# Kernel tuning notes

Hardware: AMD Instinct MI355X
Metric: run time of the kernel (lower is better)

Reference implementation:

```python
import jax, jax.numpy as jnp
import numpy as np

N = 65536        # lattice nodes (256x256 grid)
E_RAND = 1_000_000  # non-self-loop causal edges (~16 per node)
T = 65           # max edge type after add_self_loops (type 1 = self loop)
FIN = 8
FOUT = 8
B = 16           # batch of spin configurations


def setup_inputs() -> dict:
    key = jax.random.key(0)
    k1, k2, k3, k4, k5, k6 = jax.random.split(key, 6)
    x = jax.random.normal(k1, (N, FIN, B), dtype=jnp.float32)
    bound = 1.0 / np.sqrt(FIN)  # matches reset_parameters uniform init
    W = jax.random.uniform(k2, (T, FOUT, FIN), jnp.float32, -bound, bound)
    b = jax.random.uniform(k3, (T, FOUT), jnp.float32, -bound, bound)
    # add_self_loops: identity edges with type 1, other types shifted to 2..T
    loops = jnp.arange(N, dtype=jnp.int32)
    src = jnp.concatenate([loops, jax.random.randint(k4, (E_RAND,), 0, N, dtype=jnp.int32)])
    tgt = jnp.concatenate([loops, jax.random.randint(k5, (E_RAND,), 0, N, dtype=jnp.int32)])
    etype = jnp.concatenate([
        jnp.ones((N,), dtype=jnp.int32),
        jax.random.randint(k6, (E_RAND,), 2, T + 1, dtype=jnp.int32),
    ])
    return {"x": x, "W": W, "b": b, "src": src, "tgt": tgt, "etype": etype}


def reference(x, W, b, src, tgt, etype):
    # Faithful to GraphConvLayer.forward (depth=None): the expanded sparse
    # weight matrix assigns a unique [FOUT,FIN] block W[t-1] to every base
    # edge (tgt,src) of type t, and torch.sparse.mm sums duplicate entries.
    Wg = W[etype - 1]                              # [E, FOUT, FIN] gather by edge type
    msg = jnp.einsum('eoi,eib->eob', Wg, x[src])   # per-edge messages [E, FOUT, B]
    y = jax.ops.segment_sum(msg, tgt, num_segments=N)       # [N, FOUT, B]
    # bias graph expanded with source_dim=1, multiplied by ones -> per-edge bias
    yb = jax.ops.segment_sum(b[etype - 1], tgt, num_segments=N)  # [N, FOUT]
    return y + yb[:, :, None]
```

## Files before the change

### kernel.cpp

```cpp
#include <hip/hip_runtime.h>


#define CAP 48
#define ROWSTRIDE 52
#define DUMMY_T 65
#define NT 66
#define BUCKETS 512
#define BNODES 128
#define WCAP 32
#define CHUNK 4096

typedef short bf16x8 __attribute__((ext_vector_type(8)));
typedef float f32x4 __attribute__((ext_vector_type(4)));

__device__ __forceinline__ unsigned f2bf(float f) {
    unsigned u = __float_as_uint(f);
    return (u + 0x7FFFu + ((u >> 16) & 1u)) >> 16;
}

__device__ __forceinline__ int qperm(int r) { return (r == 1) ? 2 : (r == 2) ? 1 : r; }

__global__ __launch_bounds__(256)
void bin_a(const float* __restrict__ x, const float* __restrict__ W,
           const int* __restrict__ rsrc, const int* __restrict__ rtgt,
           const int* __restrict__ rety,
           int* __restrict__ cnts, unsigned* __restrict__ bdata,
           uint4* __restrict__ xt, uint4* __restrict__ Wbf, int N, int ER, int nchunk) {
    __shared__ int hist[BUCKETS];
    __shared__ int curs[BUCKETS];
    int bid = blockIdx.x, tid = threadIdx.x;

    if (bid < nchunk) {
        hist[tid] = 0; hist[tid + 256] = 0;
        curs[tid] = 0; curs[tid + 256] = 0;
        __syncthreads();
        int e0 = bid * CHUNK;
        int lim = ER - e0; if (lim > CHUNK) lim = CHUNK;

        unsigned pay[4][4];
        int bb[4][4];
        int nv[4];
#pragma unroll
        for (int g = 0; g < 4; ++g) {
            int r = tid * 4 + g * 1024;
            int n = lim - r; n = n < 0 ? 0 : (n > 4 ? 4 : n);
            nv[g] = n;
            if (n == 4) {
                int4 tv = *reinterpret_cast<const int4*>(rtgt + e0 + r);
                int4 sv = *reinterpret_cast<const int4*>(rsrc + e0 + r);
                int4 qv = *reinterpret_cast<const int4*>(rety + e0 + r);
                bb[g][0] = tv.x >> 7; pay[g][0] = (unsigned)(tv.x & 127) | ((unsigned)sv.x << 7) | ((unsigned)(qv.x - 1) << 23);
                bb[g][1] = tv.y >> 7; pay[g][1] = (unsigned)(tv.y & 127) | ((unsigned)sv.y << 7) | ((unsigned)(qv.y - 1) << 23);
                bb[g][2] = tv.z >> 7; pay[g][2] = (unsigned)(tv.z & 127) | ((unsigned)sv.z << 7) | ((unsigned)(qv.z - 1) << 23);
                bb[g][3] = tv.w >> 7; pay[g][3] = (unsigned)(tv.w & 127) | ((unsigned)sv.w << 7) | ((unsigned)(qv.w - 1) << 23);
            } else {
#pragma unroll
                for (int u = 0; u < 4; ++u) {
                    if (u < n) {
                        int e = e0 + r + u;
                        int t = rtgt[e];
                        bb[g][u] = t >> 7;
                        pay[g][u] = (unsigned)(t & 127) | ((unsigned)rsrc[e] << 7)
                                  | ((unsigned)(rety[e] - 1) << 23);
                    } else { bb[g][u] = 0; pay[g][u] = 0; }
                }
            }
#pragma unroll
            for (int u = 0; u < 4; ++u)
                if (u < nv[g]) atomicAdd(&hist[bb[g][u]], 1);
        }
        __syncthreads();
        cnts[bid * BUCKETS + tid]       = min(hist[tid], WCAP);
        cnts[bid * BUCKETS + tid + 256] = min(hist[tid + 256], WCAP);
#pragma unroll
        for (int g = 0; g < 4; ++g) {
#pragma unroll
            for (int u = 0; u < 4; ++u) {
                if (u < nv[g]) {
                    int bkt = bb[g][u];
                    int pos = atomicAdd(&curs[bkt], 1);
                    if (pos < WCAP)
                        bdata[((size_t)bkt * nchunk + bid) * WCAP + pos] = pay[g][u];
                }
            }
        }
    } else if (bid < nchunk + (N * 16) / 256) {
        int p = (bid - nchunk) * 256 + tid;
        int n = p >> 4, j = p & 15;
        const float* xp = x + (size_t)n * 128 + j;
        unsigned w[4];
#pragma unroll
        for (int i = 0; i < 4; ++i)
            w[i] = f2bf(xp[(2 * i) * 16]) | (f2bf(xp[(2 * i + 1) * 16]) << 16);
        xt[p] = make_uint4(w[0], w[1], w[2], w[3]);
    } else {
        for (int i = tid; i < NT * 8; i += 256) {
            uint4 wv = make_uint4(0, 0, 0, 0);
            if (i < 65 * 8) {
                const float* wr = W + (size_t)i * 8;
                wv = make_uint4(f2bf(wr[0]) | (f2bf(wr[1]) << 16),
                                f2bf(wr[2]) | (f2bf(wr[3]) << 16),
                                f2bf(wr[4]) | (f2bf(wr[5]) << 16),
                                f2bf(wr[6]) | (f2bf(wr[7]) << 16));
            }
            Wbf[i] = wv;
        }
    }
}

__global__ __launch_bounds__(512, 8)
void build_gather(const int* __restrict__ cnts, const unsigned* __restrict__ bdata,
                  const float* __restrict__ bias, const uint4* __restrict__ xt,
                  const uint4* __restrict__ Wbf, float* __restrict__ out, int nchunk) {
    __shared__ unsigned ladj[BNODES * ROWSTRIDE];
    __shared__ int ldeg[BNODES];
    __shared__ int lnit[BNODES];
    __shared__ float blds[NT * 8];
    __shared__ float lyb[BNODES * 8];
    __shared__ int lcnt[512];
    int b = blockIdx.x, tid = threadIdx.x;

    if (tid < BNODES) ldeg[tid] = 0;
    const unsigned DUM = (unsigned)DUMMY_T << 16;
    uint4* l4 = reinterpret_cast<uint4*>(ladj);
#pragma unroll 4
    for (int i = tid; i < BNODES * ROWSTRIDE / 4; i += 512)
        l4[i] = make_uint4(DUM, DUM, DUM, DUM);
    for (int i = tid; i < NT * 8; i += 512)
        blds[i] = (i < 65 * 8) ? bias[i] : 0.f;
    for (int i = tid; i < nchunk; i += 512)
        lcnt[i] = cnts[i * BUCKETS + b];
    __syncthreads();

    const unsigned* bp = bdata + (size_t)b * nchunk * WCAP;
    int totslots = nchunk * WCAP;
    for (int s = tid; s < totslots; s += 512) {
        int c = s >> 5, k = s & 31;
        if (k < lcnt[c]) {
            unsigned p = bp[s];
            int tl = (int)(p & 127u);
            int pos = atomicAdd(&ldeg[tl], 1);
            if (pos < CAP)
                ladj[tl * ROWSTRIDE + (pos & ~3) + qperm(pos & 3)] =
                    ((p >> 7) & 0xFFFFu) | ((p >> 23) << 16);
        }
    }
    __syncthreads();

    if (tid < BNODES) {
        int node = b * BNODES + tid;
        int d = ldeg[tid]; if (d > CAP) d = CAP;
        ladj[tid * ROWSTRIDE + (d & ~3) + qperm(d & 3)] = (unsigned)node;
        lnit[tid] = (d + 4) >> 2;
    }
    __syncthreads();

#pragma unroll
    for (int base = 0; base < BNODES * 8; base += 512) {
        int idx = base + tid;
        int nl = idx >> 3, o = idx & 7;
        int nq4 = lnit[nl] * 4;
        float yb = 0.f;
        const unsigned* row = ladj + nl * ROWSTRIDE;
        for (int k = 0; k < nq4; ++k)
            yb += blds[(row[k] >> 16) * 8 + o];
        lyb[idx] = yb;
    }
    __syncthreads();

    int lane = tid & 63;
    int wave = tid >> 6;
    int j = lane & 15;
    int h = lane >> 4;
    bool aact = ((h & 1) == 0) ? (j < 8) : (j >= 8);
    int rowoff = (h & 1) * 4;
    const float4* ybp = reinterpret_cast<const float4*>(lyb);

    for (int pp = 0; pp < 8; ++pp) {
        int nAl = (wave << 4) + (pp << 1);
        int nBl = nAl + 1;
        int nit = max(lnit[nAl], lnit[nBl]);
        const unsigned* apA = ladj + nAl * ROWSTRIDE + h;
        const unsigned* apB = ladj + nBl * ROWSTRIDE + h;

        f32x4 accA = {0.f, 0.f, 0.f, 0.f};
        f32x4 accB = {0.f, 0.f, 0.f, 0.f};

        unsigned pkA = apA[0], pkB = apB[0];
        uint4 xvA = xt[(pkA & 0xFFFFu) * 16 + j];
        uint4 xvB = xt[(pkB & 0xFFFFu) * 16 + j];
        uint4 wvA = Wbf[(aact ? (pkA >> 16) : (unsigned)DUMMY_T) * 8 + (j & 7)];
        uint4 wvB = Wbf[(aact ? (pkB >> 16) : (unsigned)DUMMY_T) * 8 + (j & 7)];

        for (int i = 1; i < nit; ++i) {
            unsigned pkA2 = apA[i * 4], pkB2 = apB[i * 4];
            uint4 xvA2 = xt[(pkA2 & 0xFFFFu) * 16 + j];
            uint4 xvB2 = xt[(pkB2 & 0xFFFFu) * 16 + j];
            uint4 wvA2 = Wbf[(aact ? (pkA2 >> 16) : (unsigned)DUMMY_T) * 8 + (j & 7)];
            uint4 wvB2 = Wbf[(aact ? (pkB2 >> 16) : (unsigned)DUMMY_T) * 8 + (j & 7)];
            accA = __builtin_amdgcn_mfma_f32_16x16x32_bf16(
                       __builtin_bit_cast(bf16x8, wvA), __builtin_bit_cast(bf16x8, xvA), accA, 0, 0, 0);
            accB = __builtin_amdgcn_mfma_f32_16x16x32_bf16(
                       __builtin_bit_cast(bf16x8, wvB), __builtin_bit_cast(bf16x8, xvB), accB, 0, 0, 0);
            xvA = xvA2; wvA = wvA2; xvB = xvB2; wvB = wvB2;
        }
        accA = __builtin_amdgcn_mfma_f32_16x16x32_bf16(
                   __builtin_bit_cast(bf16x8, wvA), __builtin_bit_cast(bf16x8, xvA), accA, 0, 0, 0);
        accB = __builtin_amdgcn_mfma_f32_16x16x32_bf16(
                   __builtin_bit_cast(bf16x8, wvB), __builtin_bit_cast(bf16x8, xvB), accB, 0, 0, 0);

#pragma unroll
        for (int q = 0; q < 4; ++q) {
            accA[q] += __shfl_xor(accA[q], 32);
            accB[q] += __shfl_xor(accB[q], 32);
        }

        if (lane < 32) {
            float4 ybA = ybp[nAl * 2 + (h & 1)];
            float4 ybB = ybp[nBl * 2 + (h & 1)];
            size_t nA = (size_t)b * BNODES + nAl;
            float* opA = out + nA * 128 + rowoff * 16 + j;
            float* opB = opA + 128;
            opA[0]  = accA[0] + ybA.x;
            opA[16] = accA[1] + ybA.y;
            opA[32] = accA[2] + ybA.z;
            opA[48] = accA[3] + ybA.w;
            opB[0]  = accB[0] + ybB.x;
            opB[16] = accB[1] + ybB.y;
            opB[32] = accB[2] + ybB.z;
            opB[48] = accB[3] + ybB.w;
        }
    }
}

extern "C" void kernel_launch(void* const* d_in, const int* in_sizes, int n_in,
                              void* d_out, int out_size, void* d_ws, size_t ws_size,
                              hipStream_t stream) {
    const float* x     = (const float*)d_in[0];
    const float* W     = (const float*)d_in[1];
    const float* bias  = (const float*)d_in[2];
    const int*   src   = (const int*)d_in[3];
    const int*   tgt   = (const int*)d_in[4];
    const int*   etype = (const int*)d_in[5];
    float*       out   = (float*)d_out;

    const int N  = out_size / 128;
    const int E  = in_sizes[3];
    const int ER = E - N;
    const int nchunk = (ER + CHUNK - 1) / CHUNK;

    char* ws = (char*)d_ws;
    uint4*    xt    = (uint4*)ws;    ws += (size_t)N * 16 * 16;
    unsigned* bdata = (unsigned*)ws; ws += (size_t)BUCKETS * nchunk * WCAP * 4;
    int*      cnts  = (int*)ws;      ws += (size_t)BUCKETS * nchunk * 4;
    uint4*    Wbf   = (uint4*)ws;

    bin_a<<<nchunk + (N * 16) / 256 + 1, 256, 0, stream>>>(
        x, W, src + N, tgt + N, etype + N, cnts, bdata, xt, Wbf, N, ER, nchunk);
    build_gather<<<BUCKETS, 512, 0, stream>>>(cnts, bdata, bias, xt, Wbf, out, nchunk);
}
```

Measured before the change: 68.96 us.

## Compact bucket storage with global atomic offsets instead of per-chunk fixed slots

Result: slower. 72.18 us (+4.7%).

```diff
diff --git a/kernel.cpp b/kernel.cpp
--- a/kernel.cpp
+++ b/kernel.cpp
@@ -7,7 +7,7 @@
 #define NT 66
 #define BUCKETS 512
 #define BNODES 128
-#define WCAP 32
+#define BCAP 2304
 #define CHUNK 4096
 
 typedef short bf16x8 __attribute__((ext_vector_type(8)));
@@ -24,10 +24,11 @@
 void bin_a(const float* __restrict__ x, const float* __restrict__ W,
            const int* __restrict__ rsrc, const int* __restrict__ rtgt,
            const int* __restrict__ rety,
-           int* __restrict__ cnts, unsigned* __restrict__ bdata,
+           int* __restrict__ gcnt, unsigned* __restrict__ bdata,
            uint4* __restrict__ xt, uint4* __restrict__ Wbf, int N, int ER, int nchunk) {
     __shared__ int hist[BUCKETS];
     __shared__ int curs[BUCKETS];
+    __shared__ int gbase[BUCKETS];
     int bid = blockIdx.x, tid = threadIdx.x;
 
     if (bid < nchunk) {
@@ -70,17 +71,19 @@
                 if (u < nv[g]) atomicAdd(&hist[bb[g][u]], 1);
         }
         __syncthreads();
-        cnts[bid * BUCKETS + tid]       = min(hist[tid], WCAP);
-        cnts[bid * BUCKETS + tid + 256] = min(hist[tid + 256], WCAP);
+        int hv = hist[tid];
+        gbase[tid] = hv ? atomicAdd(&gcnt[tid], hv) : 0;
+        hv = hist[tid + 256];
+        gbase[tid + 256] = hv ? atomicAdd(&gcnt[tid + 256], hv) : 0;
+        __syncthreads();
 #pragma unroll
         for (int g = 0; g < 4; ++g) {
 #pragma unroll
             for (int u = 0; u < 4; ++u) {
                 if (u < nv[g]) {
                     int bkt = bb[g][u];
-                    int pos = atomicAdd(&curs[bkt], 1);
-                    if (pos < WCAP)
-                        bdata[((size_t)bkt * nchunk + bid) * WCAP + pos] = pay[g][u];
+                    int pos = gbase[bkt] + atomicAdd(&curs[bkt], 1);
+                    if (pos < BCAP) bdata[(size_t)bkt * BCAP + pos] = pay[g][u];
                 }
             }
         }
@@ -109,15 +112,14 @@
 }
 
 __global__ __launch_bounds__(512, 8)
-void build_gather(const int* __restrict__ cnts, const unsigned* __restrict__ bdata,
+void build_gather(const int* __restrict__ gcnt, const unsigned* __restrict__ bdata,
                   const float* __restrict__ bias, const uint4* __restrict__ xt,
-                  const uint4* __restrict__ Wbf, float* __restrict__ out, int nchunk) {
+                  const uint4* __restrict__ Wbf, float* __restrict__ out) {
     __shared__ unsigned ladj[BNODES * ROWSTRIDE];
     __shared__ int ldeg[BNODES];
     __shared__ int lnit[BNODES];
     __shared__ float blds[NT * 8];
     __shared__ float lyb[BNODES * 8];
-    __shared__ int lcnt[512];
     int b = blockIdx.x, tid = threadIdx.x;
 
     if (tid < BNODES) ldeg[tid] = 0;
@@ -128,21 +130,24 @@
         l4[i] = make_uint4(DUM, DUM, DUM, DUM);
     for (int i = tid; i < NT * 8; i += 512)
         blds[i] = (i < 65 * 8) ? bias[i] : 0.f;
-    for (int i = tid; i < nchunk; i += 512)
-        lcnt[i] = cnts[i * BUCKETS + b];
-    __syncthreads();
-
-    const unsigned* bp = bdata + (size_t)b * nchunk * WCAP;
-    int totslots = nchunk * WCAP;
-    for (int s = tid; s < totslots; s += 512) {
-        int c = s >> 5, k = s & 31;
-        if (k < lcnt[c]) {
-            unsigned p = bp[s];
-            int tl = (int)(p & 127u);
-            int pos = atomicAdd(&ldeg[tl], 1);
-            if (pos < CAP)
-                ladj[tl * ROWSTRIDE + (pos & ~3) + qperm(pos & 3)] =
-                    ((p >> 7) & 0xFFFFu) | ((p >> 23) << 16);
+    __syncthreads();
+
+    int cnt = gcnt[b]; if (cnt > BCAP) cnt = BCAP;
+    const uint4* bp4 = reinterpret_cast<const uint4*>(bdata + (size_t)b * BCAP);
+    for (int i4 = tid; i4 * 4 < cnt; i4 += 512) {
+        uint4 pv = bp4[i4];
+        int base = i4 * 4;
+        unsigned pp[4] = {pv.x, pv.y, pv.z, pv.w};
+#pragma unroll
+        for (int u = 0; u < 4; ++u) {
+            if (base + u < cnt) {
+                unsigned p = pp[u];
+                int tl = (int)(p & 127u);
+                int pos = atomicAdd(&ldeg[tl], 1);
+                if (pos < CAP)
+                    ladj[tl * ROWSTRIDE + (pos & ~3) + qperm(pos & 3)] =
+                        ((p >> 7) & 0xFFFFu) | ((p >> 23) << 16);
+            }
         }
     }
     __syncthreads();
@@ -251,11 +256,12 @@
 
     char* ws = (char*)d_ws;
     uint4*    xt    = (uint4*)ws;    ws += (size_t)N * 16 * 16;
-    unsigned* bdata = (unsigned*)ws; ws += (size_t)BUCKETS * nchunk * WCAP * 4;
-    int*      cnts  = (int*)ws;      ws += (size_t)BUCKETS * nchunk * 4;
+    unsigned* bdata = (unsigned*)ws; ws += (size_t)BUCKETS * BCAP * 4;
+    int*      gcnt  = (int*)ws;      ws += (size_t)BUCKETS * 4;
     uint4*    Wbf   = (uint4*)ws;
 
+    hipMemsetAsync(gcnt, 0, (size_t)BUCKETS * 4, stream);
     bin_a<<<nchunk + (N * 16) / 256 + 1, 256, 0, stream>>>(
-        x, W, src + N, tgt + N, etype + N, cnts, bdata, xt, Wbf, N, ER, nchunk);
-    build_gather<<<BUCKETS, 512, 0, stream>>>(cnts, bdata, bias, xt, Wbf, out, nchunk);
-}
+        x, W, src + N, tgt + N, etype + N, gcnt, bdata, xt, Wbf, N, ER, nchunk);
+    build_gather<<<BUCKETS, 512, 0, stream>>>(gcnt, bdata, bias, xt, Wbf, out);
+}
```

## Single-pass edge binning with larger chunks and vectorized bucket reads

Applied to the files above, without the earlier changes.

Result: no change. 68.44 us (-0.8%).

```diff
diff --git a/kernel.cpp b/kernel.cpp
--- a/kernel.cpp
+++ b/kernel.cpp
@@ -7,8 +7,9 @@
 #define NT 66
 #define BUCKETS 512
 #define BNODES 128
-#define WCAP 32
-#define CHUNK 4096
+#define WCAP 48
+#define WQ (WCAP / 4)
+#define CHUNK 8192
 
 typedef short bf16x8 __attribute__((ext_vector_type(8)));
 typedef float f32x4 __attribute__((ext_vector_type(4)));
@@ -26,64 +27,47 @@
            const int* __restrict__ rety,
            int* __restrict__ cnts, unsigned* __restrict__ bdata,
            uint4* __restrict__ xt, uint4* __restrict__ Wbf, int N, int ER, int nchunk) {
-    __shared__ int hist[BUCKETS];
     __shared__ int curs[BUCKETS];
     int bid = blockIdx.x, tid = threadIdx.x;
 
     if (bid < nchunk) {
-        hist[tid] = 0; hist[tid + 256] = 0;
         curs[tid] = 0; curs[tid + 256] = 0;
         __syncthreads();
         int e0 = bid * CHUNK;
         int lim = ER - e0; if (lim > CHUNK) lim = CHUNK;
-
-        unsigned pay[4][4];
-        int bb[4][4];
-        int nv[4];
-#pragma unroll
-        for (int g = 0; g < 4; ++g) {
-            int r = tid * 4 + g * 1024;
-            int n = lim - r; n = n < 0 ? 0 : (n > 4 ? 4 : n);
-            nv[g] = n;
-            if (n == 4) {
+        for (int r = tid * 4; r < lim; r += 1024) {
+            if (r + 4 <= lim) {
                 int4 tv = *reinterpret_cast<const int4*>(rtgt + e0 + r);
                 int4 sv = *reinterpret_cast<const int4*>(rsrc + e0 + r);
                 int4 qv = *reinterpret_cast<const int4*>(rety + e0 + r);
-                bb[g][0] = tv.x >> 7; pay[g][0] = (unsigned)(tv.x & 127) | ((unsigned)sv.x << 7) | ((unsigned)(qv.x - 1) << 23);
-                bb[g][1] = tv.y >> 7; pay[g][1] = (unsigned)(tv.y & 127) | ((unsigned)sv.y << 7) | ((unsigned)(qv.y - 1) << 23);
-                bb[g][2] = tv.z >> 7; pay[g][2] = (unsigned)(tv.z & 127) | ((unsigned)sv.z << 7) | ((unsigned)(qv.z - 1) << 23);
-                bb[g][3] = tv.w >> 7; pay[g][3] = (unsigned)(tv.w & 127) | ((unsigned)sv.w << 7) | ((unsigned)(qv.w - 1) << 23);
+                int tt[4] = {tv.x, tv.y, tv.z, tv.w};
+                int ss[4] = {sv.x, sv.y, sv.z, sv.w};
+                int qq[4] = {qv.x, qv.y, qv.z, qv.w};
+#pragma unroll
+                for (int u = 0; u < 4; ++u) {
+                    int bkt = tt[u] >> 7;
+                    unsigned pay = (unsigned)(tt[u] & 127) | ((unsigned)ss[u] << 7)
+                                 | ((unsigned)(qq[u] - 1) << 23);
+                    int pos = atomicAdd(&curs[bkt], 1);
+                    if (pos < WCAP)
+                        bdata[((size_t)bkt * nchunk + bid) * WCAP + pos] = pay;
+                }
             } else {
-#pragma unroll
-                for (int u = 0; u < 4; ++u) {
-                    if (u < n) {
-                        int e = e0 + r + u;
-                        int t = rtgt[e];
-                        bb[g][u] = t >> 7;
-                        pay[g][u] = (unsigned)(t & 127) | ((unsigned)rsrc[e] << 7)
-                                  | ((unsigned)(rety[e] - 1) << 23);
-                    } else { bb[g][u] = 0; pay[g][u] = 0; }
+                for (int q = r; q < lim; ++q) {
+                    int e = e0 + q;
+                    int t = rtgt[e];
+                    int bkt = t >> 7;
+                    unsigned pay = (unsigned)(t & 127) | ((unsigned)rsrc[e] << 7)
+                                 | ((unsigned)(rety[e] - 1) << 23);
+                    int pos = atomicAdd(&curs[bkt], 1);
+                    if (pos < WCAP)
+                        bdata[((size_t)bkt * nchunk + bid) * WCAP + pos] = pay;
                 }
             }
-#pragma unroll
-            for (int u = 0; u < 4; ++u)
-                if (u < nv[g]) atomicAdd(&hist[bb[g][u]], 1);
         }
         __syncthreads();
-        cnts[bid * BUCKETS + tid]       = min(hist[tid], WCAP);
-        cnts[bid * BUCKETS + tid + 256] = min(hist[tid + 256], WCAP);
-#pragma unroll
-        for (int g = 0; g < 4; ++g) {
-#pragma unroll
-            for (int u = 0; u < 4; ++u) {
-                if (u < nv[g]) {
-                    int bkt = bb[g][u];
-                    int pos = atomicAdd(&curs[bkt], 1);
-                    if (pos < WCAP)
-                        bdata[((size_t)bkt * nchunk + bid) * WCAP + pos] = pay[g][u];
-                }
-            }
-        }
+        cnts[bid * BUCKETS + tid]       = min(curs[tid], WCAP);
+        cnts[bid * BUCKETS + tid + 256] = min(curs[tid + 256], WCAP);
     } else if (bid < nchunk + (N * 16) / 256) {
         int p = (bid - nchunk) * 256 + tid;
         int n = p >> 4, j = p & 15;
@@ -117,7 +101,7 @@
     __shared__ int lnit[BNODES];
     __shared__ float blds[NT * 8];
     __shared__ float lyb[BNODES * 8];
-    __shared__ int lcnt[512];
+    __shared__ int lcnt[256];
     int b = blockIdx.x, tid = threadIdx.x;
 
     if (tid < BNODES) ldeg[tid] = 0;
@@ -132,17 +116,26 @@
         lcnt[i] = cnts[i * BUCKETS + b];
     __syncthreads();
 
-    const unsigned* bp = bdata + (size_t)b * nchunk * WCAP;
-    int totslots = nchunk * WCAP;
-    for (int s = tid; s < totslots; s += 512) {
-        int c = s >> 5, k = s & 31;
-        if (k < lcnt[c]) {
-            unsigned p = bp[s];
-            int tl = (int)(p & 127u);
-            int pos = atomicAdd(&ldeg[tl], 1);
-            if (pos < CAP)
-                ladj[tl * ROWSTRIDE + (pos & ~3) + qperm(pos & 3)] =
-                    ((p >> 7) & 0xFFFFu) | ((p >> 23) << 16);
+    const uint4* bp4 = reinterpret_cast<const uint4*>(bdata + (size_t)b * nchunk * WCAP);
+    int nquads = nchunk * WQ;
+    for (int s = tid; s < nquads; s += 512) {
+        int c = s / WQ;
+        int base = (s - c * WQ) * 4;
+        int cn = lcnt[c];
+        if (base < cn) {
+            uint4 pv = bp4[s];
+            unsigned pp[4] = {pv.x, pv.y, pv.z, pv.w};
+#pragma unroll
+            for (int u = 0; u < 4; ++u) {
+                if (base + u < cn) {
+                    unsigned p = pp[u];
+                    int tl = (int)(p & 127u);
+                    int pos = atomicAdd(&ldeg[tl], 1);
+                    if (pos < CAP)
+                        ladj[tl * ROWSTRIDE + (pos & ~3) + qperm(pos & 3)] =
+                            ((p >> 7) & 0xFFFFu) | ((p >> 23) << 16);
+                }
+            }
         }
     }
     __syncthreads();
```
